# Kernel tuning notes

Measured on AMD Instinct MI355X. Metric: run time of the kernel, lower is better.

The kernel has to match this reference:

```python
import jax, jax.numpy as jnp
import numpy as np

B, S, D, H, DH = 2, 2048, 1024, 16, 64
GLOBAL_RATIO = 0.1
LN_EPS = 1e-5


def setup_inputs() -> dict:
    key = jax.random.key(0)
    ks = jax.random.split(key, 8)
    w = lambda k, shape: jax.random.normal(k, shape, jnp.float32) * 0.02
    return {
        'x': jax.random.normal(ks[0], (B, S, D), jnp.float32),
        'Wq': w(ks[1], (D, H * DH)),
        'Wk': w(ks[2], (D, H * DH)),
        'Wv': w(ks[3], (D, H * DH)),
        'Wo': w(ks[4], (H * DH, D)),
        'bo': jnp.zeros((D,), jnp.float32),
        'ln_gamma': jnp.ones((DH,), jnp.float32),
        'ln_beta': jnp.zeros((DH,), jnp.float32),
        'Wg': w(ks[5], (2 * DH, DH)),
        'bg': jnp.zeros((DH,), jnp.float32),
    }


def _layernorm(x, gamma, beta):
    mu = jnp.mean(x, axis=-1, keepdims=True)
    var = jnp.mean(jnp.square(x - mu), axis=-1, keepdims=True)
    return (x - mu) * jax.lax.rsqrt(var + LN_EPS) * gamma + beta


def reference(x, Wq, Wk, Wv, Wo, bo, ln_gamma, ln_beta, Wg, bg):
    b, s, _ = x.shape
    # projections -> [b, h, n, d]
    split = lambda t: t.reshape(b, s, H, DH).transpose(0, 2, 1, 3)
    q = split(x @ Wq)
    k = split(x @ Wk)
    v = split(x @ Wv)
    scale = DH ** -0.5

    # local (full) attention: manual QK^T / softmax / AV
    scores = jnp.einsum('bhnd,bhmd->bhnm', q, k) * scale  # [b,h,s,s]
    attn = jax.nn.softmax(scores, axis=-1)
    local_out = jnp.einsum('bhnm,bhmd->bhnd', attn, v)

    # cross-segment fusion: top-k keys by norm per (b, h)
    num_global = max(1, int(s * GLOBAL_RATIO))
    key_norms = jnp.linalg.norm(k, axis=-1)  # [b,h,s]
    _, top_idx = jax.lax.top_k(key_norms, num_global)  # [b,h,g]
    idx = top_idx[..., None]  # [b,h,g,1]
    global_k = jnp.take_along_axis(k, idx, axis=2)  # [b,h,g,d]
    global_v = jnp.take_along_axis(v, idx, axis=2)
    g_scores = jnp.einsum('bhnd,bhgd->bhng', q, global_k) * scale
    g_attn = jax.nn.softmax(g_scores, axis=-1)
    global_out = jnp.einsum('bhng,bhgd->bhnd', g_attn, global_v)
    global_out = _layernorm(global_out, ln_gamma, ln_beta)

    # learned gate over [local, global]
    cat = jnp.concatenate([local_out, global_out], axis=-1)  # [b,h,s,2d]
    gate = jax.nn.sigmoid(cat @ Wg + bg)
    fused = gate * local_out + (1.0 - gate) * global_out

    out = fused.transpose(0, 2, 1, 3).reshape(b, s, H * DH)  # b h n d -> b n (h d)
    return out @ Wo + bo
```

## Files before the change

### kernel.cpp

```cpp
#include <hip/hip_runtime.h>


constexpr int SEQ    = 2048;
constexpr int DMODEL = 1024;
constexpr int NH     = 16;
constexpr int DHEAD  = 64;
constexpr int BHT    = 32;
constexpr int NG     = 204;
constexpr int NGPAD  = 256;
constexpr float LNEPS = 1e-5f;

typedef __attribute__((ext_vector_type(8))) short short8;
typedef __attribute__((ext_vector_type(4))) short short4v;
typedef __attribute__((ext_vector_type(4))) float f32x4;

__device__ __forceinline__ unsigned short f2bf(float f) {
    unsigned int u = __float_as_uint(f);
    u += 0x7FFFu + ((u >> 16) & 1u);
    return (unsigned short)(u >> 16);
}
__device__ __forceinline__ float bf2f(unsigned short b) {
    return __uint_as_float(((unsigned int)b) << 16);
}

__global__ __launch_bounds__(256)
void prep_k(const float* __restrict__ x,
            const float* __restrict__ Wq, const float* __restrict__ Wv,
            const float* __restrict__ Wo, const float* __restrict__ Wk,
            const float* __restrict__ Wg,
            unsigned short* __restrict__ xh, unsigned short* __restrict__ xl,
            unsigned short* __restrict__ Wqt, unsigned short* __restrict__ Wvt,
            unsigned short* __restrict__ Wot, unsigned short* __restrict__ Wkh,
            unsigned short* __restrict__ Wkl, unsigned short* __restrict__ Wgt)
{
    const int bid = blockIdx.x;
    const int tid = threadIdx.x;

    if (bid < 2048) {
        int i = (bid * 256 + tid) << 3;
        short8 h, l;
#pragma unroll
        for (int j = 0; j < 8; ++j) {
            float v = x[i + j];
            unsigned short hb = f2bf(v);
            h[j] = (short)hb;
            l[j] = (short)f2bf(v - bf2f(hb));
        }
        *(short8*)(xh + i) = h;
        *(short8*)(xl + i) = l;
        return;
    }
    if (bid == 3072) {
#pragma unroll
        for (int i = 0; i < 32; ++i) {
            int o = tid * 32 + i;
            int dg = o >> 7, jj = o & 127;
            Wgt[o] = f2bf(Wg[jj * 64 + dg]);
        }
        return;
    }

    __shared__ float tile[64][68];
    const int sub = bid - 2048;
    const int which = sub >> 8;
    const int b = sub & 255;
    const int n0 = (b & 15) * 64, k0 = (b >> 4) * 64;
    const float* W = (which == 0) ? Wq : (which == 1) ? Wv : (which == 2) ? Wo : Wk;
    const int Kd = DMODEL, Nd = DMODEL;

#pragma unroll
    for (int p = 0; p < 4; ++p) {
        int c = tid + (p << 8);
        int r = c >> 4, c4 = (c & 15) << 2;
        *(float4*)&tile[r][c4] = *(const float4*)(W + (size_t)(k0 + r) * Nd + n0 + c4);
    }
    __syncthreads();
#pragma unroll
    for (int p = 0; p < 4; ++p) {
        int c = tid + (p << 8);
        int n = c >> 4, k4 = (c & 15) << 2;
        if (which < 3) {
            unsigned short* Wt = (which == 0) ? Wqt : (which == 1) ? Wvt : Wot;
            short4v o;
#pragma unroll
            for (int j = 0; j < 4; ++j) o[j] = (short)f2bf(tile[k4 + j][n]);
            *(short4v*)(Wt + (size_t)(n0 + n) * Kd + k0 + k4) = o;
        } else {
            short4v oh, ol;
#pragma unroll
            for (int j = 0; j < 4; ++j) {
                float v = tile[k4 + j][n];
                unsigned short hb = f2bf(v);
                oh[j] = (short)hb;
                ol[j] = (short)f2bf(v - bf2f(hb));
            }
            *(short4v*)(Wkh + (size_t)(n0 + n) * Kd + k0 + k4) = oh;
            *(short4v*)(Wkl + (size_t)(n0 + n) * Kd + k0 + k4) = ol;
        }
    }
}

__global__ __launch_bounds__(512)
void gemm_bf16_k(const unsigned short* __restrict__ A,
                 const unsigned short* __restrict__ Bt,
                 const float* __restrict__ bias,
                 void* __restrict__ outv, void* __restrict__ outv2,
                 unsigned short* __restrict__ vtout,
                 int M, int N, int K, int mode)
{
    __shared__ __align__(16) unsigned short As[128][72];
    __shared__ __align__(16) unsigned short Bs[128][72];
    const int tid = threadIdx.x;
    const int lane = tid & 63, wave = tid >> 6;
    const int quad = lane >> 4, ln = lane & 15;
    const int mh = (wave >> 2) << 6;
    const int nh = (wave & 3) << 5;
    const int m0 = blockIdx.y * 128, n0 = blockIdx.x * 128;

    f32x4 acc[4][2];
#pragma unroll
    for (int i = 0; i < 4; ++i)
#pragma unroll
        for (int j = 0; j < 2; ++j) acc[i][j] = (f32x4){0.f, 0.f, 0.f, 0.f};

    short8 areg[2], breg[2];
#pragma unroll
    for (int p = 0; p < 2; ++p) {
        int c = tid + (p << 9);
        int row = c >> 3, col8 = (c & 7) << 3;
        areg[p] = *(const short8*)(A + (size_t)(m0 + row) * K + col8);
        breg[p] = *(const short8*)(Bt + (size_t)(n0 + row) * K + col8);
    }

    for (int k0 = 0; k0 < K; k0 += 64) {
        __syncthreads();
#pragma unroll
        for (int p = 0; p < 2; ++p) {
            int c = tid + (p << 9);
            int row = c >> 3, col8 = (c & 7) << 3;
            *(short8*)&As[row][col8] = areg[p];
            *(short8*)&Bs[row][col8] = breg[p];
        }
        __syncthreads();
        if (k0 + 64 < K) {
#pragma unroll
            for (int p = 0; p < 2; ++p) {
                int c = tid + (p << 9);
                int row = c >> 3, col8 = (c & 7) << 3;
                areg[p] = *(const short8*)(A + (size_t)(m0 + row) * K + k0 + 64 + col8);
                breg[p] = *(const short8*)(Bt + (size_t)(n0 + row) * K + k0 + 64 + col8);
            }
        }
#pragma unroll
        for (int ch = 0; ch < 2; ++ch) {
            short8 af[4], bf[2];
#pragma unroll
            for (int mt = 0; mt < 4; ++mt)
                af[mt] = *(const short8*)&As[mh + mt * 16 + ln][ch * 32 + quad * 8];
#pragma unroll
            for (int nt = 0; nt < 2; ++nt)
                bf[nt] = *(const short8*)&Bs[nh + nt * 16 + ln][ch * 32 + quad * 8];
#pragma unroll
            for (int mt = 0; mt < 4; ++mt)
#pragma unroll
                for (int nt = 0; nt < 2; ++nt)
                    acc[mt][nt] = __builtin_amdgcn_mfma_f32_16x16x32_bf16(
                        af[mt], bf[nt], acc[mt][nt], 0, 0, 0);
        }
    }

    if (mode == 0) {
        float* out = (float*)outv;
#pragma unroll
        for (int mt = 0; mt < 4; ++mt)
#pragma unroll
            for (int nt = 0; nt < 2; ++nt)
#pragma unroll
                for (int r = 0; r < 4; ++r) {
                    int m = m0 + mh + mt * 16 + quad * 4 + r;
                    int n = n0 + nh + nt * 16 + ln;
                    out[(size_t)m * N + n] = acc[mt][nt][r] + bias[n];
                }
    } else {
#pragma unroll
        for (int mt = 0; mt < 4; ++mt)
#pragma unroll
            for (int nt = 0; nt < 2; ++nt) {
                int n = n0 + nh + nt * 16 + ln;
                int mb = m0 + mh + mt * 16 + quad * 4;
                int b = mb >> 11, s0 = mb & (SEQ - 1);
                int d = n & 63;
                if (n < DMODEL) {
                    int h = n >> 6;
                    unsigned short* qp_ =
                        (unsigned short*)outv + ((size_t)(b * NH + h) * SEQ + s0) * DHEAD + d;
#pragma unroll
                    for (int r = 0; r < 4; ++r)
                        qp_[(size_t)r * DHEAD] = f2bf(acc[mt][nt][r] * 0.125f);
                } else {
                    int h = (n >> 6) - NH;
                    unsigned short* vp_ =
                        (unsigned short*)outv2 + ((size_t)(b * NH + h) * SEQ + s0) * DHEAD + d;
                    short4v tv;
#pragma unroll
                    for (int r = 0; r < 4; ++r) {
                        unsigned short bv = f2bf(acc[mt][nt][r]);
                        vp_[(size_t)r * DHEAD] = bv;
                        tv[r] = (short)bv;
                    }
                    *(short4v*)(vtout + ((size_t)(b * NH + h) * DHEAD + d) * SEQ + s0) = tv;
                }
            }
    }
}

__global__ __launch_bounds__(512)
void gemm_kproj_mfma(const unsigned short* __restrict__ xh,
                     const unsigned short* __restrict__ xl,
                     const unsigned short* __restrict__ Wh,
                     const unsigned short* __restrict__ Wl,
                     unsigned short* __restrict__ kout,
                     float* __restrict__ norms2)
{
    __shared__ __align__(16) unsigned short Ah[64][72];
    __shared__ __align__(16) unsigned short Al[64][72];
    __shared__ __align__(16) unsigned short Bh[128][72];
    __shared__ __align__(16) unsigned short Bl[128][72];
    const int K = DMODEL;
    const int tid = threadIdx.x;
    const int lane = tid & 63, wave = tid >> 6;
    const int quad = lane >> 4, ln = lane & 15;
    const int mh = (wave >> 1) << 4;
    const int nh = (wave & 1) << 6;
    const int m0 = blockIdx.y * 64, n0 = blockIdx.x * 128;

    f32x4 acc[4];
#pragma unroll
    for (int j = 0; j < 4; ++j) acc[j] = (f32x4){0.f, 0.f, 0.f, 0.f};

    const int arow = tid >> 3, acol8 = (tid & 7) << 3;
    short8 ahreg, alreg, bhreg[2], blreg[2];
    {
        size_t ga = (size_t)(m0 + arow) * K + acol8;
        ahreg = *(const short8*)(xh + ga);
        alreg = *(const short8*)(xl + ga);
#pragma unroll
        for (int p = 0; p < 2; ++p) {
            int c = tid + (p << 9);
            int row = c >> 3, col8 = (c & 7) << 3;
            size_t gb = (size_t)(n0 + row) * K + col8;
            bhreg[p] = *(const short8*)(Wh + gb);
            blreg[p] = *(const short8*)(Wl + gb);
        }
    }

    for (int k0 = 0; k0 < K; k0 += 64) {
        __syncthreads();
        *(short8*)&Ah[arow][acol8] = ahreg;
        *(short8*)&Al[arow][acol8] = alreg;
#pragma unroll
        for (int p = 0; p < 2; ++p) {
            int c = tid + (p << 9);
            int row = c >> 3, col8 = (c & 7) << 3;
            *(short8*)&Bh[row][col8] = bhreg[p];
            *(short8*)&Bl[row][col8] = blreg[p];
        }
        __syncthreads();
        if (k0 + 64 < K) {
            size_t ga = (size_t)(m0 + arow) * K + k0 + 64 + acol8;
            ahreg = *(const short8*)(xh + ga);
            alreg = *(const short8*)(xl + ga);
#pragma unroll
            for (int p = 0; p < 2; ++p) {
                int c = tid + (p << 9);
                int row = c >> 3, col8 = (c & 7) << 3;
                size_t gb = (size_t)(n0 + row) * K + k0 + 64 + col8;
                bhreg[p] = *(const short8*)(Wh + gb);
                blreg[p] = *(const short8*)(Wl + gb);
            }
        }
#pragma unroll
        for (int ch = 0; ch < 2; ++ch) {
            short8 bh4[4], bl4[4];
#pragma unroll
            for (int nt = 0; nt < 4; ++nt) {
                bh4[nt] = *(const short8*)&Bh[nh + nt * 16 + ln][ch * 32 + quad * 8];
                bl4[nt] = *(const short8*)&Bl[nh + nt * 16 + ln][ch * 32 + quad * 8];
            }
            short8 ah = *(const short8*)&Ah[mh + ln][ch * 32 + quad * 8];
            short8 al = *(const short8*)&Al[mh + ln][ch * 32 + quad * 8];
#pragma unroll
            for (int nt = 0; nt < 4; ++nt) {
                acc[nt] = __builtin_amdgcn_mfma_f32_16x16x32_bf16(ah, bh4[nt], acc[nt], 0, 0, 0);
                acc[nt] = __builtin_amdgcn_mfma_f32_16x16x32_bf16(ah, bl4[nt], acc[nt], 0, 0, 0);
                acc[nt] = __builtin_amdgcn_mfma_f32_16x16x32_bf16(al, bh4[nt], acc[nt], 0, 0, 0);
            }
        }
    }

    const int h = (n0 + nh) >> 6;
#pragma unroll
    for (int r = 0; r < 4; ++r) {
        int m = m0 + mh + quad * 4 + r;
        int b = m >> 11, s = m & (SEQ - 1);
        size_t rowbase = ((size_t)(b * NH + h) * SEQ + s) * DHEAD;
#pragma unroll
        for (int nt = 0; nt < 4; ++nt)
            kout[rowbase + nt * 16 + ln] = f2bf(acc[nt][r]);
        float s2 = acc[0][r] * acc[0][r] + acc[1][r] * acc[1][r] +
                   acc[2][r] * acc[2][r] + acc[3][r] * acc[3][r];
#pragma unroll
        for (int off = 1; off <= 8; off <<= 1)
            s2 += __shfl_xor(s2, off);
        if (ln == 0)
            norms2[(size_t)(b * NH + h) * SEQ + s] = s2;
    }
}

__global__ __launch_bounds__(512)
void topk_gather_k(const float* __restrict__ norms2,
                   const unsigned short* __restrict__ k,
                   const unsigned short* __restrict__ v,
                   unsigned short* __restrict__ gk,
                   unsigned short* __restrict__ gvt)
{
    __shared__ unsigned long long keys[SEQ];
    __shared__ int tix[NGPAD];
    __shared__ __align__(16) unsigned short T[64][72];
    const int bh = blockIdx.x;
    const int tid = threadIdx.x;
    const float* nb = norms2 + (size_t)bh * SEQ;
    const size_t base = (size_t)bh * SEQ * DHEAD;

    for (int i = tid; i < SEQ; i += 512) {
        float nrm = sqrtf(nb[i]);
        keys[i] = ((unsigned long long)__float_as_uint(nrm) << 32) |
                  (unsigned int)(0xFFFFFFFFu - (unsigned int)i);
    }
    __syncthreads();
    for (int kk = 2; kk <= SEQ; kk <<= 1) {
        for (int j = kk >> 1; j > 0; j >>= 1) {
            for (int i = tid; i < SEQ; i += 512) {
                int ixj = i ^ j;
                if (ixj > i) {
                    unsigned long long a = keys[i], b = keys[ixj];
                    bool up = ((i & kk) == 0);
                    if ((a > b) == up) { keys[i] = b; keys[ixj] = a; }
                }
            }
            __syncthreads();
        }
    }
    if (tid < NGPAD) {
        tix[tid] = (tid < NG)
            ? (int)(0xFFFFFFFFu - (unsigned int)(keys[SEQ - 1 - tid] & 0xFFFFFFFFu))
            : 0;
    }
    __syncthreads();

    for (int t = 0; t < NGPAD / 64; ++t) {
        {
            int idx = tid;
            int row = idx >> 3, col8 = (idx & 7) << 3;
            int g = t * 64 + row;
            short8 kv = (short8)0, vv = (short8)0;
            if (g < NG) {
                int sidx = tix[g];
                kv = *(const short8*)(k + base + (size_t)sidx * DHEAD + col8);
                vv = *(const short8*)(v + base + (size_t)sidx * DHEAD + col8);
            }
            *(short8*)(gk + ((size_t)bh * NGPAD + g) * DHEAD + col8) = kv;
            *(short8*)&T[row][col8] = vv;
        }
        __syncthreads();
        {
            int idx = tid;
            int d = idx >> 3, k8 = (idx & 7) << 3;
            short8 o;
#pragma unroll
            for (int i = 0; i < 8; ++i) o[i] = (short)T[k8 + i][d];
            *(short8*)(gvt + ((size_t)bh * DHEAD + d) * NGPAD + t * 64 + k8) = o;
        }
        __syncthreads();
    }
}

__global__ __launch_bounds__(256, 2)
void attn_fused_k(const unsigned short* __restrict__ qb,
                  const unsigned short* __restrict__ kb,
                  const unsigned short* __restrict__ vt,
                  const unsigned short* __restrict__ gk,
                  const unsigned short* __restrict__ gvt,
                  const unsigned short* __restrict__ Wgt,
                  const float* __restrict__ gamma,
                  const float* __restrict__ beta,
                  const float* __restrict__ bg,
                  unsigned short* __restrict__ fused)
{
    __shared__ __align__(16) unsigned short Ks[64][72];
    __shared__ __align__(16) unsigned short Vt[64][72];
    __shared__ __align__(16) unsigned short Ps[128][72];
    __shared__ __align__(16) unsigned short Wgs[64][136];
    const int flat = blockIdx.x;
    const int bh = ((flat >> 7) << 3) | (flat & 7);
    const int q0 = ((flat >> 3) & 15) * 128;
    const int tid = threadIdx.x;
    const int lane = tid & 63, wave = tid >> 6;
    const int quad = lane >> 4, ln = lane & 15;
    const size_t base = (size_t)bh * SEQ * DHEAD;
    const unsigned short* gkb = gk + (size_t)bh * NGPAD * DHEAD;
    const unsigned short* gvb = gvt + (size_t)bh * DHEAD * NGPAD;

#pragma unroll
    for (int p = 0; p < 4; ++p) {
        int idx = tid + (p << 8);
        *(short8*)&Wgs[idx >> 4][(idx & 15) << 3] = *(const short8*)(Wgt + idx * 8);
    }

    short8 qf[2][2];
#pragma unroll
    for (int mt = 0; mt < 2; ++mt) {
        const unsigned short* qp = qb + base + (size_t)(q0 + wave * 32 + mt * 16 + ln) * DHEAD;
        qf[mt][0] = *(const short8*)(qp + quad * 8);
        qf[mt][1] = *(const short8*)(qp + 32 + quad * 8);
    }

    f32x4 O[2][4], Og[2][4];
#pragma unroll
    for (int mt = 0; mt < 2; ++mt)
#pragma unroll
        for (int nt = 0; nt < 4; ++nt) {
            O[mt][nt] = (f32x4){0.f, 0.f, 0.f, 0.f};
            Og[mt][nt] = (f32x4){0.f, 0.f, 0.f, 0.f};
        }
    float ls[2] = {0.f, 0.f}, lg[2] = {0.f, 0.f};

    short8 kreg[2], vreg[2];
    int srow[2], scol8[2];
#pragma unroll
    for (int p = 0; p < 2; ++p) {
        int idx = tid + (p << 8);
        srow[p] = idx >> 3;
        scol8[p] = (idx & 7) << 3;
        kreg[p] = *(const short8*)(kb + base + (size_t)srow[p] * DHEAD + scol8[p]);
        vreg[p] = *(const short8*)(vt + base + (size_t)srow[p] * SEQ + scol8[p]);
    }

    for (int t = 0; t < SEQ / 64; ++t) {
        __syncthreads();
#pragma unroll
        for (int p = 0; p < 2; ++p) {
            *(short8*)&Ks[srow[p]][scol8[p]] = kreg[p];
            *(short8*)&Vt[srow[p]][scol8[p]] = vreg[p];
        }
        __syncthreads();
        if (t + 1 < SEQ / 64) {
#pragma unroll
            for (int p = 0; p < 2; ++p) {
                kreg[p] = *(const short8*)(kb + base + (size_t)((t + 1) * 64 + srow[p]) * DHEAD + scol8[p]);
                vreg[p] = *(const short8*)(vt + base + (size_t)srow[p] * SEQ + (t + 1) * 64 + scol8[p]);
            }
        } else {
#pragma unroll
            for (int p = 0; p < 2; ++p) {
                kreg[p] = *(const short8*)(gkb + (size_t)srow[p] * DHEAD + scol8[p]);
                vreg[p] = *(const short8*)(gvb + (size_t)srow[p] * NGPAD + scol8[p]);
            }
        }

        f32x4 s[2][4];
#pragma unroll
        for (int mt = 0; mt < 2; ++mt)
#pragma unroll
            for (int nt = 0; nt < 4; ++nt) s[mt][nt] = (f32x4){0.f, 0.f, 0.f, 0.f};
        __builtin_amdgcn_s_setprio(1);
#pragma unroll
        for (int nt = 0; nt < 4; ++nt) {
            short8 kf0 = *(const short8*)&Ks[nt * 16 + ln][quad * 8];
            short8 kf1 = *(const short8*)&Ks[nt * 16 + ln][32 + quad * 8];
#pragma unroll
            for (int mt = 0; mt < 2; ++mt) {
                s[mt][nt] = __builtin_amdgcn_mfma_f32_16x16x32_bf16(kf0, qf[mt][0], s[mt][nt], 0, 0, 0);
                s[mt][nt] = __builtin_amdgcn_mfma_f32_16x16x32_bf16(kf1, qf[mt][1], s[mt][nt], 0, 0, 0);
            }
        }
        __builtin_amdgcn_s_setprio(0);

        short4v pf[2][4];
#pragma unroll
        for (int mt = 0; mt < 2; ++mt)
#pragma unroll
            for (int nt = 0; nt < 4; ++nt)
#pragma unroll
                for (int r = 0; r < 4; ++r) {
                    unsigned int u = __float_as_uint(__expf(s[mt][nt][r]));
                    ls[mt] += __uint_as_float(u & 0xFFFF0000u);
                    pf[mt][nt][r] = (short)(u >> 16);
                }

        __builtin_amdgcn_s_setprio(1);
#pragma unroll
        for (int dt = 0; dt < 4; ++dt)
#pragma unroll
            for (int ks = 0; ks < 4; ++ks) {
                short4v vf = *(const short4v*)&Vt[dt * 16 + ln][ks * 16 + quad * 4];
#pragma unroll
                for (int mt = 0; mt < 2; ++mt)
                    O[mt][dt] = __builtin_amdgcn_mfma_f32_16x16x16bf16_1k(
                        pf[mt][ks], vf, O[mt][dt], 0, 0, 0);
            }
        __builtin_amdgcn_s_setprio(0);
    }

    for (int t = 0; t < NGPAD / 64; ++t) {
        __syncthreads();
#pragma unroll
        for (int p = 0; p < 2; ++p) {
            *(short8*)&Ks[srow[p]][scol8[p]] = kreg[p];
            *(short8*)&Vt[srow[p]][scol8[p]] = vreg[p];
        }
        __syncthreads();
        if (t + 1 < NGPAD / 64) {
#pragma unroll
            for (int p = 0; p < 2; ++p) {
                kreg[p] = *(const short8*)(gkb + (size_t)((t + 1) * 64 + srow[p]) * DHEAD + scol8[p]);
                vreg[p] = *(const short8*)(gvb + (size_t)srow[p] * NGPAD + (t + 1) * 64 + scol8[p]);
            }
        }

        f32x4 s[2][4];
#pragma unroll
        for (int mt = 0; mt < 2; ++mt)
#pragma unroll
            for (int nt = 0; nt < 4; ++nt) s[mt][nt] = (f32x4){0.f, 0.f, 0.f, 0.f};
        __builtin_amdgcn_s_setprio(1);
#pragma unroll
        for (int nt = 0; nt < 4; ++nt) {
            short8 kf0 = *(const short8*)&Ks[nt * 16 + ln][quad * 8];
            short8 kf1 = *(const short8*)&Ks[nt * 16 + ln][32 + quad * 8];
#pragma unroll
            for (int mt = 0; mt < 2; ++mt) {
                s[mt][nt] = __builtin_amdgcn_mfma_f32_16x16x32_bf16(kf0, qf[mt][0], s[mt][nt], 0, 0, 0);
                s[mt][nt] = __builtin_amdgcn_mfma_f32_16x16x32_bf16(kf1, qf[mt][1], s[mt][nt], 0, 0, 0);
            }
        }
        __builtin_amdgcn_s_setprio(0);

        short4v pf[2][4];
#pragma unroll
        for (int nt = 0; nt < 4; ++nt)
#pragma unroll
            for (int r = 0; r < 4; ++r) {
                bool valid = (t * 64 + nt * 16 + quad * 4 + r) < NG;
#pragma unroll
                for (int mt = 0; mt < 2; ++mt) {
                    float p = valid ? __expf(s[mt][nt][r]) : 0.f;
                    unsigned int u = __float_as_uint(p);
                    lg[mt] += __uint_as_float(u & 0xFFFF0000u);
                    pf[mt][nt][r] = (short)(u >> 16);
                }
            }

        __builtin_amdgcn_s_setprio(1);
#pragma unroll
        for (int dt = 0; dt < 4; ++dt)
#pragma unroll
            for (int ks = 0; ks < 4; ++ks) {
                short4v vf = *(const short4v*)&Vt[dt * 16 + ln][ks * 16 + quad * 4];
#pragma unroll
                for (int mt = 0; mt < 2; ++mt)
                    Og[mt][dt] = __builtin_amdgcn_mfma_f32_16x16x16bf16_1k(
                        pf[mt][ks], vf, Og[mt][dt], 0, 0, 0);
            }
        __builtin_amdgcn_s_setprio(0);
    }

#pragma unroll
    for (int mt = 0; mt < 2; ++mt) {
        ls[mt] += __shfl_xor(ls[mt], 16);
        ls[mt] += __shfl_xor(ls[mt], 32);
        lg[mt] += __shfl_xor(lg[mt], 16);
        lg[mt] += __shfl_xor(lg[mt], 32);
    }
    float invl[2][4], invg[2][4];
#pragma unroll
    for (int mt = 0; mt < 2; ++mt)
#pragma unroll
        for (int r = 0; r < 4; ++r) {
            invl[mt][r] = 1.f / __shfl(ls[mt], quad * 4 + r);
            invg[mt][r] = 1.f / __shfl(lg[mt], quad * 4 + r);
        }

    float xs[2][4][4];
#pragma unroll
    for (int mt = 0; mt < 2; ++mt)
#pragma unroll
        for (int r = 0; r < 4; ++r) {
            float inv = invg[mt][r];
#pragma unroll
            for (int nt = 0; nt < 4; ++nt) xs[mt][nt][r] = Og[mt][nt][r] * inv;
        }
    float mu[2][4], rsd[2][4];
#pragma unroll
    for (int mt = 0; mt < 2; ++mt)
#pragma unroll
        for (int r = 0; r < 4; ++r) {
            float sm = xs[mt][0][r] + xs[mt][1][r] + xs[mt][2][r] + xs[mt][3][r];
#pragma unroll
            for (int off = 1; off <= 8; off <<= 1) sm += __shfl_xor(sm, off);
            mu[mt][r] = sm * (1.f / 64.f);
        }
#pragma unroll
    for (int mt = 0; mt < 2; ++mt)
#pragma unroll
        for (int r = 0; r < 4; ++r) {
            float sv = 0.f;
#pragma unroll
            for (int nt = 0; nt < 4; ++nt) {
                float d = xs[mt][nt][r] - mu[mt][r];
                sv += d * d;
            }
#pragma unroll
            for (int off = 1; off <= 8; off <<= 1) sv += __shfl_xor(sv, off);
            rsd[mt][r] = rsqrtf(sv * (1.f / 64.f) + LNEPS);
        }
#pragma unroll
    for (int nt = 0; nt < 4; ++nt) {
        float g = gamma[nt * 16 + ln], bb = beta[nt * 16 + ln];
#pragma unroll
        for (int mt = 0; mt < 2; ++mt)
#pragma unroll
            for (int r = 0; r < 4; ++r)
                xs[mt][nt][r] = (xs[mt][nt][r] - mu[mt][r]) * rsd[mt][r] * g + bb;
    }

    float lf[2][4][4];
#pragma unroll
    for (int mt = 0; mt < 2; ++mt)
#pragma unroll
        for (int nt = 0; nt < 4; ++nt)
#pragma unroll
            for (int r = 0; r < 4; ++r) {
                lf[mt][nt][r] = O[mt][nt][r] * invl[mt][r];
                Ps[wave * 32 + mt * 16 + quad * 4 + r][nt * 16 + ln] = f2bf(lf[mt][nt][r]);
            }
    f32x4 gacc[2][4];
#pragma unroll
    for (int ng = 0; ng < 4; ++ng) {
        float bgv = bg[ng * 16 + ln];
#pragma unroll
        for (int mt = 0; mt < 2; ++mt)
            gacc[mt][ng] = (f32x4){bgv, bgv, bgv, bgv};
    }
#pragma unroll
    for (int ch = 0; ch < 2; ++ch) {
        short8 af[2];
#pragma unroll
        for (int mt = 0; mt < 2; ++mt)
            af[mt] = *(const short8*)&Ps[wave * 32 + mt * 16 + ln][ch * 32 + quad * 8];
#pragma unroll
        for (int ng = 0; ng < 4; ++ng) {
            short8 bf = *(const short8*)&Wgs[ng * 16 + ln][ch * 32 + quad * 8];
#pragma unroll
            for (int mt = 0; mt < 2; ++mt)
                gacc[mt][ng] = __builtin_amdgcn_mfma_f32_16x16x32_bf16(af[mt], bf, gacc[mt][ng], 0, 0, 0);
        }
    }
#pragma unroll
    for (int mt = 0; mt < 2; ++mt)
#pragma unroll
        for (int nt = 0; nt < 4; ++nt)
#pragma unroll
            for (int r = 0; r < 4; ++r)
                Ps[wave * 32 + mt * 16 + quad * 4 + r][nt * 16 + ln] = f2bf(xs[mt][nt][r]);
#pragma unroll
    for (int ch = 0; ch < 2; ++ch) {
        short8 af[2];
#pragma unroll
        for (int mt = 0; mt < 2; ++mt)
            af[mt] = *(const short8*)&Ps[wave * 32 + mt * 16 + ln][ch * 32 + quad * 8];
#pragma unroll
        for (int ng = 0; ng < 4; ++ng) {
            short8 bf = *(const short8*)&Wgs[ng * 16 + ln][64 + ch * 32 + quad * 8];
#pragma unroll
            for (int mt = 0; mt < 2; ++mt)
                gacc[mt][ng] = __builtin_amdgcn_mfma_f32_16x16x32_bf16(af[mt], bf, gacc[mt][ng], 0, 0, 0);
        }
    }

    const int b = bh >> 4, h = bh & 15;
#pragma unroll
    for (int mt = 0; mt < 2; ++mt)
#pragma unroll
        for (int ng = 0; ng < 4; ++ng)
#pragma unroll
            for (int r = 0; r < 4; ++r) {
                float gt = 1.f / (1.f + __expf(-gacc[mt][ng][r]));
                float f = gt * lf[mt][ng][r] + (1.f - gt) * xs[mt][ng][r];
                int s = q0 + wave * 32 + mt * 16 + quad * 4 + r;
                fused[((size_t)(b * SEQ + s)) * DMODEL + h * DHEAD + ng * 16 + ln] = f2bf(f);
            }
}

extern "C" void kernel_launch(void* const* d_in, const int* in_sizes, int n_in,
                              void* d_out, int out_size, void* d_ws, size_t ws_size,
                              hipStream_t stream)
{
    (void)in_sizes; (void)n_in; (void)out_size; (void)ws_size;
    const float* x    = (const float*)d_in[0];
    const float* Wq   = (const float*)d_in[1];
    const float* Wk   = (const float*)d_in[2];
    const float* Wv   = (const float*)d_in[3];
    const float* Wo   = (const float*)d_in[4];
    const float* bo   = (const float*)d_in[5];
    const float* ln_g = (const float*)d_in[6];
    const float* ln_b = (const float*)d_in[7];
    const float* Wg   = (const float*)d_in[8];
    const float* bg   = (const float*)d_in[9];

    char* w = (char*)d_ws;
    const size_t MB = 1024ull * 1024ull;
    unsigned short* kb16  = (unsigned short*)(w);
    unsigned short* qb16  = (unsigned short*)(w + 8 * MB);
    unsigned short* vb16  = (unsigned short*)(w + 16 * MB);
    unsigned short* vt16  = (unsigned short*)(w + 24 * MB);
    unsigned short* xh    = (unsigned short*)(w + 32 * MB);
    unsigned short* xl    = (unsigned short*)(w + 40 * MB);
    unsigned short* Wqt   = (unsigned short*)(w + 48 * MB);
    unsigned short* Wvt   = (unsigned short*)(w + 50 * MB);
    unsigned short* Wot   = (unsigned short*)(w + 52 * MB);
    unsigned short* Wkh   = (unsigned short*)(w + 54 * MB);
    unsigned short* Wkl   = (unsigned short*)(w + 56 * MB);
    unsigned short* Wgt   = (unsigned short*)(w + 58 * MB);
    float*          norms2= (float*)(w + 59 * MB);
    unsigned short* gk16  = (unsigned short*)(w + 60 * MB);
    unsigned short* gvt16 = (unsigned short*)(w + 61 * MB);
    unsigned short* fusedb = xh;

    const int M = 4096, N = 1024, K = 1024;

    prep_k<<<3073, 256, 0, stream>>>(x, Wq, Wv, Wo, Wk, Wg,
                                     xh, xl, Wqt, Wvt, Wot, Wkh, Wkl, Wgt);

    dim3 gqv(2048 / 128, M / 128);
    gemm_bf16_k<<<gqv, 512, 0, stream>>>(xh, Wqt, nullptr, qb16, vb16, vt16,
                                         M, 2048, K, 3);

    dim3 gkp(N / 128, M / 64);
    gemm_kproj_mfma<<<gkp, 512, 0, stream>>>(xh, xl, Wkh, Wkl, kb16, norms2);

    topk_gather_k<<<BHT, 512, 0, stream>>>(norms2, kb16, vb16, gk16, gvt16);

    attn_fused_k<<<512, 256, 0, stream>>>(qb16, kb16, vt16, gk16, gvt16, Wgt,
                                          ln_g, ln_b, bg, fusedb);

    dim3 go_(N / 128, M / 128);
    gemm_bf16_k<<<go_, 512, 0, stream>>>(fusedb, Wot, bo, (float*)d_out, nullptr,
                                         nullptr, M, N, K, 0);
}
```

Baseline: 280.2 us.

## Double-buffer K/V tiles in LDS and fold log2e into Q scale for exp2

Replaces the single K/V shared tile with a two-slot ring buffer. Each tile's store to LDS now happens after compute, with a prefetch two tiles ahead, so each iteration needs one barrier instead of two. Shared memory is unioned so Ps aliases the K/V buffers and total LDS stays bounded. Separately, the Q scale now includes log2(e), so the softmax uses exp2f instead of __expf, saving a multiply per element.

Result: slower. 300.5 us (+7.2%).

```diff
diff --git a/kernel.cpp b/kernel.cpp
--- a/kernel.cpp
+++ b/kernel.cpp
@@ -196,7 +196,7 @@
                         (unsigned short*)outv + ((size_t)(b * NH + h) * SEQ + s0) * DHEAD + d;
 #pragma unroll
                     for (int r = 0; r < 4; ++r)
-                        qp_[(size_t)r * DHEAD] = f2bf(acc[mt][nt][r] * 0.125f);
+                        qp_[(size_t)r * DHEAD] = f2bf(acc[mt][nt][r] * 0.18033688f);
                 } else {
                     int h = (n >> 6) - NH;
                     unsigned short* vp_ =
@@ -397,10 +397,12 @@
                   const float* __restrict__ bg,
                   unsigned short* __restrict__ fused)
 {
-    __shared__ __align__(16) unsigned short Ks[64][72];
-    __shared__ __align__(16) unsigned short Vt[64][72];
-    __shared__ __align__(16) unsigned short Ps[128][72];
-    __shared__ __align__(16) unsigned short Wgs[64][136];
+    __shared__ __align__(16) unsigned short smem[27136];
+    unsigned short* const KsB = smem;
+    unsigned short* const VtB = smem + 9216;
+    unsigned short (*Ps)[72]  = (unsigned short (*)[72])smem;
+    unsigned short (*Wgs)[136] = (unsigned short (*)[136])(smem + 18432);
+
     const int flat = blockIdx.x;
     const int bh = ((flat >> 7) << 3) | (flat & 7);
     const int q0 = ((flat >> 3) & 15) * 128;
@@ -442,31 +444,40 @@
         int idx = tid + (p << 8);
         srow[p] = idx >> 3;
         scol8[p] = (idx & 7) << 3;
-        kreg[p] = *(const short8*)(kb + base + (size_t)srow[p] * DHEAD + scol8[p]);
-        vreg[p] = *(const short8*)(vt + base + (size_t)srow[p] * SEQ + scol8[p]);
-    }
-
-    for (int t = 0; t < SEQ / 64; ++t) {
-        __syncthreads();
+    }
+
+    auto loadT = [&](int i) {
 #pragma unroll
         for (int p = 0; p < 2; ++p) {
-            *(short8*)&Ks[srow[p]][scol8[p]] = kreg[p];
-            *(short8*)&Vt[srow[p]][scol8[p]] = vreg[p];
-        }
-        __syncthreads();
-        if (t + 1 < SEQ / 64) {
-#pragma unroll
-            for (int p = 0; p < 2; ++p) {
-                kreg[p] = *(const short8*)(kb + base + (size_t)((t + 1) * 64 + srow[p]) * DHEAD + scol8[p]);
-                vreg[p] = *(const short8*)(vt + base + (size_t)srow[p] * SEQ + (t + 1) * 64 + scol8[p]);
-            }
-        } else {
-#pragma unroll
-            for (int p = 0; p < 2; ++p) {
-                kreg[p] = *(const short8*)(gkb + (size_t)srow[p] * DHEAD + scol8[p]);
-                vreg[p] = *(const short8*)(gvb + (size_t)srow[p] * NGPAD + scol8[p]);
-            }
-        }
+            if (i < 32) {
+                kreg[p] = *(const short8*)(kb + base + (size_t)(i * 64 + srow[p]) * DHEAD + scol8[p]);
+                vreg[p] = *(const short8*)(vt + base + (size_t)srow[p] * SEQ + i * 64 + scol8[p]);
+            } else {
+                int g = i - 32;
+                kreg[p] = *(const short8*)(gkb + (size_t)(g * 64 + srow[p]) * DHEAD + scol8[p]);
+                vreg[p] = *(const short8*)(gvb + (size_t)srow[p] * NGPAD + g * 64 + scol8[p]);
+            }
+        }
+    };
+    auto storeT = [&](int buf) {
+        unsigned short* kd = KsB + buf * 4608;
+        unsigned short* vd = VtB + buf * 4608;
+#pragma unroll
+        for (int p = 0; p < 2; ++p) {
+            *(short8*)&kd[srow[p] * 72 + scol8[p]] = kreg[p];
+            *(short8*)&vd[srow[p] * 72 + scol8[p]] = vreg[p];
+        }
+    };
+
+    loadT(0);
+    storeT(0);
+    loadT(1);
+    __syncthreads();
+
+    for (int t = 0; t < 32; ++t) {
+        const int cur = t & 1;
+        const unsigned short* Kc = KsB + cur * 4608;
+        const unsigned short* Vc = VtB + cur * 4608;
 
         f32x4 s[2][4];
 #pragma unroll
@@ -476,8 +487,8 @@
         __builtin_amdgcn_s_setprio(1);
 #pragma unroll
         for (int nt = 0; nt < 4; ++nt) {
-            short8 kf0 = *(const short8*)&Ks[nt * 16 + ln][quad * 8];
-            short8 kf1 = *(const short8*)&Ks[nt * 16 + ln][32 + quad * 8];
+            short8 kf0 = *(const short8*)&Kc[(nt * 16 + ln) * 72 + quad * 8];
+            short8 kf1 = *(const short8*)&Kc[(nt * 16 + ln) * 72 + 32 + quad * 8];
 #pragma unroll
             for (int mt = 0; mt < 2; ++mt) {
                 s[mt][nt] = __builtin_amdgcn_mfma_f32_16x16x32_bf16(kf0, qf[mt][0], s[mt][nt], 0, 0, 0);
@@ -493,7 +504,7 @@
             for (int nt = 0; nt < 4; ++nt)
 #pragma unroll
                 for (int r = 0; r < 4; ++r) {
-                    unsigned int u = __float_as_uint(__expf(s[mt][nt][r]));
+                    unsigned int u = __float_as_uint(exp2f(s[mt][nt][r]));
                     ls[mt] += __uint_as_float(u & 0xFFFF0000u);
                     pf[mt][nt][r] = (short)(u >> 16);
                 }
@@ -503,30 +514,24 @@
         for (int dt = 0; dt < 4; ++dt)
 #pragma unroll
             for (int ks = 0; ks < 4; ++ks) {
-                short4v vf = *(const short4v*)&Vt[dt * 16 + ln][ks * 16 + quad * 4];
+                short4v vf = *(const short4v*)&Vc[(dt * 16 + ln) * 72 + ks * 16 + quad * 4];
 #pragma unroll
                 for (int mt = 0; mt < 2; ++mt)
                     O[mt][dt] = __builtin_amdgcn_mfma_f32_16x16x16bf16_1k(
                         pf[mt][ks], vf, O[mt][dt], 0, 0, 0);
             }
         __builtin_amdgcn_s_setprio(0);
-    }
-
-    for (int t = 0; t < NGPAD / 64; ++t) {
+
+        storeT(cur ^ 1);
+        if (t + 2 <= 35) loadT(t + 2);
         __syncthreads();
-#pragma unroll
-        for (int p = 0; p < 2; ++p) {
-            *(short8*)&Ks[srow[p]][scol8[p]] = kreg[p];
-            *(short8*)&Vt[srow[p]][scol8[p]] = vreg[p];
-        }
-        __syncthreads();
-        if (t + 1 < NGPAD / 64) {
-#pragma unroll
-            for (int p = 0; p < 2; ++p) {
-                kreg[p] = *(const short8*)(gkb + (size_t)((t + 1) * 64 + srow[p]) * DHEAD + scol8[p]);
-                vreg[p] = *(const short8*)(gvb + (size_t)srow[p] * NGPAD + (t + 1) * 64 + scol8[p]);
-            }
-        }
+    }
+
+    for (int tg = 0; tg < 4; ++tg) {
+        const int t = 32 + tg;
+        const int cur = t & 1;
+        const unsigned short* Kc = KsB + cur * 4608;
+        const unsigned short* Vc = VtB + cur * 4608;
 
         f32x4 s[2][4];
 #pragma unroll
@@ -536,8 +541,8 @@
         __builtin_amdgcn_s_setprio(1);
 #pragma unroll
         for (int nt = 0; nt < 4; ++nt) {
-            short8 kf0 = *(const short8*)&Ks[nt * 16 + ln][quad * 8];
-            short8 kf1 = *(const short8*)&Ks[nt * 16 + ln][32 + quad * 8];
+            short8 kf0 = *(const short8*)&Kc[(nt * 16 + ln) * 72 + quad * 8];
+            short8 kf1 = *(const short8*)&Kc[(nt * 16 + ln) * 72 + 32 + quad * 8];
 #pragma unroll
             for (int mt = 0; mt < 2; ++mt) {
                 s[mt][nt] = __builtin_amdgcn_mfma_f32_16x16x32_bf16(kf0, qf[mt][0], s[mt][nt], 0, 0, 0);
@@ -551,10 +556,10 @@
         for (int nt = 0; nt < 4; ++nt)
 #pragma unroll
             for (int r = 0; r < 4; ++r) {
-                bool valid = (t * 64 + nt * 16 + quad * 4 + r) < NG;
+                bool valid = (tg * 64 + nt * 16 + quad * 4 + r) < NG;
 #pragma unroll
                 for (int mt = 0; mt < 2; ++mt) {
-                    float p = valid ? __expf(s[mt][nt][r]) : 0.f;
+                    float p = valid ? exp2f(s[mt][nt][r]) : 0.f;
                     unsigned int u = __float_as_uint(p);
                     lg[mt] += __uint_as_float(u & 0xFFFF0000u);
                     pf[mt][nt][r] = (short)(u >> 16);
@@ -566,13 +571,17 @@
         for (int dt = 0; dt < 4; ++dt)
 #pragma unroll
             for (int ks = 0; ks < 4; ++ks) {
-                short4v vf = *(const short4v*)&Vt[dt * 16 + ln][ks * 16 + quad * 4];
+                short4v vf = *(const short4v*)&Vc[(dt * 16 + ln) * 72 + ks * 16 + quad * 4];
 #pragma unroll
                 for (int mt = 0; mt < 2; ++mt)
                     Og[mt][dt] = __builtin_amdgcn_mfma_f32_16x16x16bf16_1k(
                         pf[mt][ks], vf, Og[mt][dt], 0, 0, 0);
             }
         __builtin_amdgcn_s_setprio(0);
+
+        if (t < 35) storeT(cur ^ 1);
+        if (t + 2 <= 35) loadT(t + 2);
+        __syncthreads();
     }
 
 #pragma unroll
```
